# Optimization experiments

Measured on AMD Instinct MI355X. Metric: run time of the kernel, lower is better.

The kernel has to match this reference:

```python
import jax, jax.numpy as jnp
import numpy as np

NUM_HEADS = 32
NUM_KV_HEADS = 8
HEAD_DIM = 128


def setup_inputs() -> dict:
    key = jax.random.key(0)
    ks = jax.random.split(key, 5)
    B, S, H = 2, 2048, 4096
    Dq = NUM_HEADS * HEAD_DIM      # 4096
    Dkv = NUM_KV_HEADS * HEAD_DIM  # 1024
    return {
        "hidden_states": jax.random.normal(ks[0], (B, S, H), jnp.float32),
        "w_q": jax.random.normal(ks[1], (H, Dq), jnp.float32) * 0.02,
        "w_k": jax.random.normal(ks[2], (H, Dkv), jnp.float32) * 0.02,
        "w_v": jax.random.normal(ks[3], (H, Dkv), jnp.float32) * 0.02,
        "w_o": jax.random.normal(ks[4], (Dq, H), jnp.float32) * 0.02,
    }


def reference(hidden_states, w_q, w_k, w_v, w_o):
    # GQA causal attention, prefill path (no KV cache, RoPE is a no-op in source).
    B, S, _ = hidden_states.shape
    Hq, Hkv, D = NUM_HEADS, NUM_KV_HEADS, HEAD_DIM
    g = Hq // Hkv  # kv groups
    scale = D ** -0.5

    q = (hidden_states @ w_q).reshape(B, S, Hkv, g, D)  # [B,S,Hkv,g,D]
    k = (hidden_states @ w_k).reshape(B, S, Hkv, D)     # [B,S,Hkv,D]
    v = (hidden_states @ w_v).reshape(B, S, Hkv, D)

    # repeat_kv expressed as grouped einsum (avoids materializing repeated K/V)
    scores = jnp.einsum('bqhgd,bkhd->bhgqk', q, k) * scale  # [B,Hkv,g,S,S]
    causal = jnp.tril(jnp.ones((S, S), dtype=bool))
    scores = jnp.where(causal, scores, -jnp.inf)
    probs = jax.nn.softmax(scores.astype(jnp.float32), axis=-1).astype(q.dtype)

    attn = jnp.einsum('bhgqk,bkhd->bqhgd', probs, v)  # [B,S,Hkv,g,D]
    attn = attn.reshape(B, S, Hq * D)
    return attn @ w_o
```

## Files before the change

kernel.cpp:

```cpp
#include <hip/hip_runtime.h>

typedef unsigned short u16;
typedef __attribute__((ext_vector_type(8))) short bf16x8;
typedef __attribute__((ext_vector_type(8))) unsigned short u16x8;
typedef __attribute__((ext_vector_type(4))) unsigned short u16x4;
typedef __attribute__((ext_vector_type(4))) float f32x4;

__device__ __forceinline__ u16 f2bf(float f) {
  union { float f; unsigned u; } v; v.f = f;
  unsigned r = v.u + 0x7fffu + ((v.u >> 16) & 1u);
  return (u16)(r >> 16);
}

__device__ __forceinline__ void gload16(const u16* g, u16* l) {
  __builtin_amdgcn_global_load_lds((const __attribute__((address_space(1))) void*)g,
                                   (__attribute__((address_space(3))) void*)l, 16, 0, 0);
}

__global__ __launch_bounds__(256) void cast_bf16_kern(const float* __restrict__ in,
                                                      u16* __restrict__ out, int n) {
  int i = (blockIdx.x * 256 + threadIdx.x) * 8;
  if (i >= n) return;
  float4 a = *(const float4*)(in + i);
  float4 b = *(const float4*)(in + i + 4);
  u16x8 r;
  r[0] = f2bf(a.x); r[1] = f2bf(a.y); r[2] = f2bf(a.z); r[3] = f2bf(a.w);
  r[4] = f2bf(b.x); r[5] = f2bf(b.y); r[6] = f2bf(b.z); r[7] = f2bf(b.w);
  *(u16x8*)(out + i) = r;
}

__global__ __launch_bounds__(256) void transpose_cast_kern(const float* __restrict__ in,
                                                           u16* __restrict__ out, int K, int N) {
  __shared__ float tile[64][65];
  int nbx = N >> 6;
  int n0 = (blockIdx.x % nbx) << 6;
  int k0 = (blockIdx.x / nbx) << 6;
  int tx = threadIdx.x & 15;
  int ty = threadIdx.x >> 4;
#pragma unroll
  for (int r = 0; r < 64; r += 16) {
    float4 v = *(const float4*)(in + (size_t)(k0 + ty + r) * N + n0 + tx * 4);
    tile[ty + r][tx * 4 + 0] = v.x;
    tile[ty + r][tx * 4 + 1] = v.y;
    tile[ty + r][tx * 4 + 2] = v.z;
    tile[ty + r][tx * 4 + 3] = v.w;
  }
  __syncthreads();
#pragma unroll
  for (int r = 0; r < 64; r += 16) {
    u16x4 o;
#pragma unroll
    for (int j = 0; j < 4; j++) o[j] = f2bf(tile[tx * 4 + j][ty + r]);
    *(u16x4*)(out + (size_t)(n0 + ty + r) * K + k0 + tx * 4) = o;
  }
}

#define PH_PRE()                                           \
  asm volatile("" ::: "memory");                           \
  __builtin_amdgcn_s_barrier();                            \
  asm volatile("" ::: "memory");                           \
  __builtin_amdgcn_s_setprio(1)

#define PH_POST()                                          \
  __builtin_amdgcn_s_setprio(0);                           \
  asm volatile("" ::: "memory");                           \
  __builtin_amdgcn_s_barrier();                            \
  asm volatile("" ::: "memory")

template <int MODE>
__global__ __launch_bounds__(512, 2) void gemm256(const u16* __restrict__ A,
                                                  const u16* __restrict__ Bt,
                                                  void* __restrict__ Cout,
                                                  int M, int N, int K) {
  __shared__ u16 lds[65536];
  const int tid = threadIdx.x;
  const int lane = tid & 63, w = tid >> 6;
  const int wm = w >> 2, wn = w & 3;
  const int li = lane & 15, lg = lane >> 4;
  const int NT = K >> 6;

  const int nbx = N >> 8;
  const int nwg = gridDim.x;
  const int swz = (blockIdx.x & 7) * (nwg >> 3) + (blockIdx.x >> 3);
  const int m0 = (swz / nbx) << 8;
  const int n0 = (swz % nbx) << 8;

  const int srow = w * 16 + (lane >> 3);
  const int scol = ((lane & 7) ^ (lane >> 3)) << 3;
  const u16* sA0 = A + (size_t)(m0 + srow) * K + scol;
  const u16* sA1 = A + (size_t)(m0 + 128 + srow) * K + scol;
  const u16* sB0 = Bt + (size_t)(n0 + srow) * K + scol;
  const u16* sB1 = Bt + (size_t)(n0 + 128 + srow) * K + scol;
  const size_t jK = (size_t)8 * K;
  u16* dA0 = lds + w * 1024;
  u16* dA1 = lds + 8192 + w * 1024;
  u16* dB0 = lds + 32768 + w * 1024;
  u16* dB1 = lds + 32768 + 8192 + w * 1024;

#define STG(sp, dp, t_) do {                                          \
    int db_ = (t_) & 1;                                               \
    gload16((sp) + (size_t)(t_) * 64, (dp) + db_ * 16384);            \
    gload16((sp) + (size_t)(t_) * 64 + jK, (dp) + db_ * 16384 + 512); \
  } while (0)

  STG(sA0, dA0, 0); STG(sA1, dA1, 0); STG(sB0, dB0, 0); STG(sB1, dB1, 0);
  STG(sA0, dA0, 1); STG(sA1, dA1, 1); STG(sB0, dB0, 1); STG(sB1, dB1, 1);
  asm volatile("s_waitcnt vmcnt(8)" ::: "memory");
  __builtin_amdgcn_s_barrier();
  asm volatile("" ::: "memory");

  f32x4 acc[8][4];
#pragma unroll
  for (int m = 0; m < 8; m++)
#pragma unroll
    for (int n = 0; n < 4; n++) acc[m][n] = (f32x4){0.f, 0.f, 0.f, 0.f};

  const int xsw = (li & 7) << 3;
  const int k0o = (lg * 8) ^ xsw;
  const int k1o = (32 + lg * 8) ^ xsw;
  const u16* aBase = lds + wm * 8192;
  const u16* bBase = lds + 32768 + (wn >> 1) * 8192;
  const int brow0 = (wn & 1) * 64;

  bf16x8 a[4][2], b[4][2];

  for (int t = 0; t < NT; ++t) {
    const int db = t & 1;
    const u16* Ab = aBase + db * 16384;
    const u16* Bb = bBase + db * 16384;

#pragma unroll
    for (int mf = 0; mf < 4; mf++) {
      int r = mf * 16 + li;
      a[mf][0] = *(const bf16x8*)(Ab + r * 64 + k0o);
      a[mf][1] = *(const bf16x8*)(Ab + r * 64 + k1o);
    }
#pragma unroll
    for (int nf = 0; nf < 2; nf++) {
      int r = brow0 + nf * 16 + li;
      b[nf][0] = *(const bf16x8*)(Bb + r * 64 + k0o);
      b[nf][1] = *(const bf16x8*)(Bb + r * 64 + k1o);
    }
    PH_PRE();
#pragma unroll
    for (int mf = 0; mf < 4; mf++)
#pragma unroll
      for (int nf = 0; nf < 2; nf++) {
        acc[mf][nf] = __builtin_amdgcn_mfma_f32_16x16x32_bf16(a[mf][0], b[nf][0], acc[mf][nf], 0, 0, 0);
        acc[mf][nf] = __builtin_amdgcn_mfma_f32_16x16x32_bf16(a[mf][1], b[nf][1], acc[mf][nf], 0, 0, 0);
      }
    PH_POST();

#pragma unroll
    for (int nf = 2; nf < 4; nf++) {
      int r = brow0 + nf * 16 + li;
      b[nf][0] = *(const bf16x8*)(Bb + r * 64 + k0o);
      b[nf][1] = *(const bf16x8*)(Bb + r * 64 + k1o);
    }
    PH_PRE();
#pragma unroll
    for (int mf = 0; mf < 4; mf++)
#pragma unroll
      for (int nf = 2; nf < 4; nf++) {
        acc[mf][nf] = __builtin_amdgcn_mfma_f32_16x16x32_bf16(a[mf][0], b[nf][0], acc[mf][nf], 0, 0, 0);
        acc[mf][nf] = __builtin_amdgcn_mfma_f32_16x16x32_bf16(a[mf][1], b[nf][1], acc[mf][nf], 0, 0, 0);
      }
    PH_POST();

#pragma unroll
    for (int mf = 0; mf < 4; mf++) {
      int r = (mf + 4) * 16 + li;
      a[mf][0] = *(const bf16x8*)(Ab + r * 64 + k0o);
      a[mf][1] = *(const bf16x8*)(Ab + r * 64 + k1o);
    }
    if (t + 2 < NT) { STG(sB0, dB0, t + 2); STG(sB1, dB1, t + 2); }
    PH_PRE();
#pragma unroll
    for (int mf = 0; mf < 4; mf++)
#pragma unroll
      for (int nf = 2; nf < 4; nf++) {
        acc[mf + 4][nf] = __builtin_amdgcn_mfma_f32_16x16x32_bf16(a[mf][0], b[nf][0], acc[mf + 4][nf], 0, 0, 0);
        acc[mf + 4][nf] = __builtin_amdgcn_mfma_f32_16x16x32_bf16(a[mf][1], b[nf][1], acc[mf + 4][nf], 0, 0, 0);
      }
    PH_POST();

    if (t + 2 < NT) { STG(sA0, dA0, t + 2); STG(sA1, dA1, t + 2); }
    PH_PRE();
#pragma unroll
    for (int mf = 0; mf < 4; mf++)
#pragma unroll
      for (int nf = 0; nf < 2; nf++) {
        acc[mf + 4][nf] = __builtin_amdgcn_mfma_f32_16x16x32_bf16(a[mf][0], b[nf][0], acc[mf + 4][nf], 0, 0, 0);
        acc[mf + 4][nf] = __builtin_amdgcn_mfma_f32_16x16x32_bf16(a[mf][1], b[nf][1], acc[mf + 4][nf], 0, 0, 0);
      }
    __builtin_amdgcn_s_setprio(0);
    if (t < NT - 2) {
      asm volatile("s_waitcnt vmcnt(8)" ::: "memory");
    } else {
      asm volatile("s_waitcnt vmcnt(0)" ::: "memory");
    }
    __builtin_amdgcn_s_barrier();
    asm volatile("" ::: "memory");
  }

#pragma unroll
  for (int mf = 0; mf < 8; mf++)
#pragma unroll
    for (int nf = 0; nf < 4; nf++)
#pragma unroll
      for (int r = 0; r < 4; r++) {
        int gm = m0 + wm * 128 + mf * 16 + lg * 4 + r;
        int gn = n0 + wn * 64 + nf * 16 + li;
        if (MODE == 0)
          ((u16*)Cout)[(size_t)gm * N + gn] = f2bf(acc[mf][nf][r]);
        else
          ((float*)Cout)[(size_t)gm * N + gn] = acc[mf][nf][r];
      }
#undef STG
}

__global__ __launch_bounds__(512, 2) void gemm_kv(const u16* __restrict__ A,
                                                  const u16* __restrict__ Bt,
                                                  u16* __restrict__ Kout,
                                                  u16* __restrict__ Vout) {
  __shared__ u16 lds[49152];
  const int tid = threadIdx.x;
  const int lane = tid & 63, w = tid >> 6;
  const int wm = w >> 2, wn = w & 3;
  const int li = lane & 15, lg = lane >> 4;
  const int K = 4096, NT = 64;

  const int swz = (blockIdx.x & 7) * 32 + (blockIdx.x >> 3);
  const int m0 = (swz >> 3) << 7;
  const int n0 = (swz & 7) << 8;

  const int srow = w * 16 + (lane >> 3);
  const int scol = ((lane & 7) ^ (lane >> 3)) << 3;
  const u16* sA  = A  + (size_t)(m0 + srow) * K + scol;
  const u16* sB0 = Bt + (size_t)(n0 + srow) * K + scol;
  const u16* sB1 = Bt + (size_t)(n0 + 128 + srow) * K + scol;
  const size_t jK = (size_t)8 * K;
  u16* dA  = lds + w * 1024;
  u16* dB0 = lds + 16384 + w * 1024;
  u16* dB1 = lds + 16384 + 8192 + w * 1024;

#define STGA(t_) do { int db_ = (t_) & 1;                                     \
    gload16(sA + (size_t)(t_) * 64, dA + db_ * 8192);                         \
    gload16(sA + (size_t)(t_) * 64 + jK, dA + db_ * 8192 + 512); } while (0)
#define STGB(t_) do { int db_ = (t_) & 1;                                     \
    gload16(sB0 + (size_t)(t_) * 64, dB0 + db_ * 16384);                      \
    gload16(sB0 + (size_t)(t_) * 64 + jK, dB0 + db_ * 16384 + 512);           \
    gload16(sB1 + (size_t)(t_) * 64, dB1 + db_ * 16384);                      \
    gload16(sB1 + (size_t)(t_) * 64 + jK, dB1 + db_ * 16384 + 512); } while (0)

  STGA(0); STGB(0); STGB(1);
  asm volatile("s_waitcnt vmcnt(4)" ::: "memory");
  __builtin_amdgcn_s_barrier();
  asm volatile("" ::: "memory");

  f32x4 acc[4][4];
#pragma unroll
  for (int m = 0; m < 4; m++)
#pragma unroll
    for (int n = 0; n < 4; n++) acc[m][n] = (f32x4){0.f, 0.f, 0.f, 0.f};

  const int xsw = (li & 7) << 3;
  const int k0o = (lg * 8) ^ xsw;
  const int k1o = (32 + lg * 8) ^ xsw;
  const int arow0 = wm * 64;
  const u16* bBase0 = lds + 16384 + (wn >> 1) * 8192;
  const int brow0 = (wn & 1) * 64;

  bf16x8 a[4][2], b[4][2];

  for (int t = 0; t < NT; ++t) {
    const int db = t & 1;
    const u16* Ab = lds + db * 8192;
    const u16* Bb = bBase0 + db * 16384;

#pragma unroll
    for (int mf = 0; mf < 2; mf++) {
      int r = arow0 + mf * 16 + li;
      a[mf][0] = *(const bf16x8*)(Ab + r * 64 + k0o);
      a[mf][1] = *(const bf16x8*)(Ab + r * 64 + k1o);
    }
#pragma unroll
    for (int nf = 0; nf < 4; nf++) {
      int r = brow0 + nf * 16 + li;
      b[nf][0] = *(const bf16x8*)(Bb + r * 64 + k0o);
      b[nf][1] = *(const bf16x8*)(Bb + r * 64 + k1o);
    }
    if (t + 1 < NT) STGA(t + 1);
    PH_PRE();
#pragma unroll
    for (int mf = 0; mf < 2; mf++)
#pragma unroll
      for (int nf = 0; nf < 4; nf++) {
        acc[mf][nf] = __builtin_amdgcn_mfma_f32_16x16x32_bf16(a[mf][0], b[nf][0], acc[mf][nf], 0, 0, 0);
        acc[mf][nf] = __builtin_amdgcn_mfma_f32_16x16x32_bf16(a[mf][1], b[nf][1], acc[mf][nf], 0, 0, 0);
      }
    PH_POST();

#pragma unroll
    for (int mf = 2; mf < 4; mf++) {
      int r = arow0 + mf * 16 + li;
      a[mf][0] = *(const bf16x8*)(Ab + r * 64 + k0o);
      a[mf][1] = *(const bf16x8*)(Ab + r * 64 + k1o);
    }
    if (t + 2 < NT) STGB(t + 2);
    PH_PRE();
#pragma unroll
    for (int mf = 2; mf < 4; mf++)
#pragma unroll
      for (int nf = 0; nf < 4; nf++) {
        acc[mf][nf] = __builtin_amdgcn_mfma_f32_16x16x32_bf16(a[mf][0], b[nf][0], acc[mf][nf], 0, 0, 0);
        acc[mf][nf] = __builtin_amdgcn_mfma_f32_16x16x32_bf16(a[mf][1], b[nf][1], acc[mf][nf], 0, 0, 0);
      }
    __builtin_amdgcn_s_setprio(0);
    if (t < NT - 2) {
      asm volatile("s_waitcnt vmcnt(4)" ::: "memory");
    } else {
      asm volatile("s_waitcnt vmcnt(0)" ::: "memory");
    }
    __builtin_amdgcn_s_barrier();
    asm volatile("" ::: "memory");
  }

#pragma unroll
  for (int mf = 0; mf < 4; mf++)
#pragma unroll
    for (int nf = 0; nf < 4; nf++)
#pragma unroll
      for (int r = 0; r < 4; r++) {
        int gm = m0 + wm * 64 + mf * 16 + lg * 4 + r;
        int gn = n0 + wn * 64 + nf * 16 + li;
        float val = acc[mf][nf][r];
        if (gn < 1024) {
          Kout[(size_t)gm * 1024 + gn] = f2bf(val);
        } else {
          int c = gn - 1024;
          int b = gm >> 11, s = gm & 2047, kvh = c >> 7, d = c & 127;
          int s2 = (s & ~31) | (((s >> 2) & 3) << 3) | (((s >> 4) & 1) << 2) | (s & 3);
          Vout[(size_t)((b * 8 + kvh) * 128 + d) * 2048 + s2] = f2bf(val);
        }
      }
#undef STGA
#undef STGB
}

__global__ __launch_bounds__(256, 2) void flash_attn_kern(const u16* __restrict__ Qg,
                                                          const u16* __restrict__ Kg,
                                                          const u16* __restrict__ VT,
                                                          u16* __restrict__ Og) {
  const int bid = blockIdx.x;
  const int qt = 63 - (bid >> 4);
  const int gh = bid & 15;
  const int b = gh >> 3, kvh = gh & 7;
  const int tid = threadIdx.x;
  const int lane = tid & 63, w = tid >> 6;
  const int li = lane & 15, lg = lane >> 4;
  const int h = kvh * 4 + w;
  const int q0 = qt << 5;
  const int nt = (qt >> 1) + 1;

  __shared__ u16 Kbuf[2][8192];
  __shared__ u16 Vbuf[2][8192];

  bf16x8 qf[2][4];
  {
    const u16* qp = Qg + ((size_t)(b * 2048 + q0 + li)) * 4096 + h * 128 + lg * 8;
#pragma unroll
    for (int m = 0; m < 2; m++)
#pragma unroll
      for (int ks = 0; ks < 4; ks++)
        qf[m][ks] = *(const bf16x8*)(qp + (size_t)(m * 16) * 4096 + ks * 32);
  }

  const u16* ksrc[4];
  const u16* vsrc[4];
#pragma unroll
  for (int i = 0; i < 4; i++) {
    int c = w * 4 + i;
    int krow = c * 4 + (lane >> 4);
    int kinner = ((lane & 15) * 16) ^ ((krow & 7) << 4);
    ksrc[i] = Kg + (size_t)(b * 2048 + krow) * 1024 + kvh * 128 + (kinner >> 1);
    int vrow = c * 8 + (lane >> 3);
    int vinner = ((lane & 7) * 16) ^ ((vrow & 7) << 4);
    vsrc[i] = VT + (size_t)((b * 8 + kvh) * 128 + vrow) * 2048 + (vinner >> 1);
  }
#pragma unroll
  for (int i = 0; i < 4; i++) {
    int c = w * 4 + i;
    gload16(ksrc[i], &Kbuf[0][c * 512]);
    gload16(vsrc[i], &Vbuf[0][c * 512]);
    ksrc[i] += 64 * 1024;
    vsrc[i] += 64;
  }

  f32x4 oa[2][8];
#pragma unroll
  for (int m = 0; m < 2; m++)
#pragma unroll
    for (int n = 0; n < 8; n++) oa[m][n] = (f32x4){0.f, 0.f, 0.f, 0.f};
  f32x4 lacc[2];
  lacc[0] = (f32x4){0.f, 0.f, 0.f, 0.f};
  lacc[1] = (f32x4){0.f, 0.f, 0.f, 0.f};
  float mrun[2] = {-1e30f, -1e30f};

  const float scale = 0.08838834764831845f;
  bf16x8 onesf;
#pragma unroll
  for (int j = 0; j < 8; j++) onesf[j] = (short)0x3F80;

  asm volatile("s_waitcnt vmcnt(0)\n\ts_barrier" ::: "memory");

  for (int t = 0; t < nt; ++t) {
    const int cur = t & 1;
    const u16* KB = Kbuf[cur];
    const u16* VB = Vbuf[cur];
    if (t + 1 < nt) {
#pragma unroll
      for (int i = 0; i < 4; i++) {
        int c = w * 4 + i;
        gload16(ksrc[i], &Kbuf[cur ^ 1][c * 512]);
        gload16(vsrc[i], &Vbuf[cur ^ 1][c * 512]);
        ksrc[i] += 64 * 1024;
        vsrc[i] += 64;
      }
    }

    f32x4 sacc[2][4];
#pragma unroll
    for (int m = 0; m < 2; m++)
#pragma unroll
      for (int n = 0; n < 4; n++) sacc[m][n] = (f32x4){0.f, 0.f, 0.f, 0.f};
    __builtin_amdgcn_s_setprio(1);
#pragma unroll
    for (int n = 0; n < 4; n++) {
      int krow = n * 16 + li;
      const u16* kb = KB + krow * 128;
      int sw = (krow & 7) << 4;
#pragma unroll
      for (int ks = 0; ks < 4; ks++) {
        bf16x8 kf = *(const bf16x8*)(kb + (((ks * 64 + lg * 16) ^ sw) >> 1));
        sacc[0][n] = __builtin_amdgcn_mfma_f32_16x16x32_bf16(kf, qf[0][ks], sacc[0][n], 0, 0, 0);
        sacc[1][n] = __builtin_amdgcn_mfma_f32_16x16x32_bf16(kf, qf[1][ks], sacc[1][n], 0, 0, 0);
      }
    }
    __builtin_amdgcn_s_setprio(0);

#pragma unroll
    for (int m = 0; m < 2; m++)
#pragma unroll
      for (int n = 0; n < 4; n++)
#pragma unroll
        for (int r = 0; r < 4; r++) sacc[m][n][r] *= scale;
    if (t == nt - 1) {
      const int kv0 = t * 64;
#pragma unroll
      for (int m = 0; m < 2; m++) {
        int q = q0 + m * 16 + li;
#pragma unroll
        for (int n = 0; n < 4; n++)
#pragma unroll
          for (int r = 0; r < 4; r++)
            if (kv0 + n * 16 + lg * 4 + r > q) sacc[m][n][r] = -1e30f;
      }
    }

#pragma unroll
    for (int m = 0; m < 2; m++) {
      float mx = sacc[m][0][0];
#pragma unroll
      for (int n = 0; n < 4; n++)
#pragma unroll
        for (int r = 0; r < 4; r++) mx = fmaxf(mx, sacc[m][n][r]);
      mx = fmaxf(mx, __shfl_xor(mx, 16, 64));
      mx = fmaxf(mx, __shfl_xor(mx, 32, 64));
      float mnew = fmaxf(mrun[m], mx);
      float corr = __expf(mrun[m] - mnew);
      mrun[m] = mnew;
#pragma unroll
      for (int n = 0; n < 4; n++)
#pragma unroll
        for (int r = 0; r < 4; r++) sacc[m][n][r] = __expf(sacc[m][n][r] - mnew);
#pragma unroll
      for (int r = 0; r < 4; r++) lacc[m][r] *= corr;
#pragma unroll
      for (int n = 0; n < 8; n++)
#pragma unroll
        for (int r = 0; r < 4; r++) oa[m][n][r] *= corr;
    }

    bf16x8 pf[2][2];
#pragma unroll
    for (int m = 0; m < 2; m++)
#pragma unroll
      for (int kvs = 0; kvs < 2; kvs++) {
        u16x8 pw;
#pragma unroll
        for (int e = 0; e < 8; e++) pw[e] = f2bf(sacc[m][2 * kvs + (e >> 2)][e & 3]);
        pf[m][kvs] = *(bf16x8*)&pw;
      }

    __builtin_amdgcn_s_setprio(1);
#pragma unroll
    for (int kvs = 0; kvs < 2; kvs++) {
#pragma unroll
      for (int n = 0; n < 8; n++) {
        int vrow = n * 16 + li;
        bf16x8 vf = *(const bf16x8*)(VB + vrow * 64 +
                                     (((kvs * 64 + lg * 16) ^ ((vrow & 7) << 4)) >> 1));
        oa[0][n] = __builtin_amdgcn_mfma_f32_16x16x32_bf16(vf, pf[0][kvs], oa[0][n], 0, 0, 0);
        oa[1][n] = __builtin_amdgcn_mfma_f32_16x16x32_bf16(vf, pf[1][kvs], oa[1][n], 0, 0, 0);
      }
      lacc[0] = __builtin_amdgcn_mfma_f32_16x16x32_bf16(onesf, pf[0][kvs], lacc[0], 0, 0, 0);
      lacc[1] = __builtin_amdgcn_mfma_f32_16x16x32_bf16(onesf, pf[1][kvs], lacc[1], 0, 0, 0);
    }
    __builtin_amdgcn_s_setprio(0);

    asm volatile("s_waitcnt vmcnt(0)\n\ts_barrier" ::: "memory");
  }

#pragma unroll
  for (int m = 0; m < 2; m++) {
    float inv = 1.0f / lacc[m][0];
    u16* op = Og + (size_t)(b * 2048 + q0 + m * 16 + li) * 4096 + h * 128 + lg * 4;
#pragma unroll
    for (int n = 0; n < 8; n++) {
      u16x4 o;
#pragma unroll
      for (int r = 0; r < 4; r++) o[r] = f2bf(oa[m][n][r] * inv);
      *(u16x4*)(op + n * 16) = o;
    }
  }
}

extern "C" void kernel_launch(void* const* d_in, const int* in_sizes, int n_in,
                              void* d_out, int out_size, void* d_ws, size_t ws_size,
                              hipStream_t stream) {
  (void)in_sizes; (void)n_in; (void)out_size; (void)ws_size;
  const float* hs = (const float*)d_in[0];
  const float* wq = (const float*)d_in[1];
  const float* wk = (const float*)d_in[2];
  const float* wv = (const float*)d_in[3];
  const float* wo = (const float*)d_in[4];

  u16* ws   = (u16*)d_ws;
  u16* hs_b = ws;
  u16* wqT  = hs_b + 16777216;
  u16* wkT  = wqT + 16777216;
  u16* wvT  = wkT + 4194304;
  u16* woT  = wvT + 4194304;
  u16* Qb   = woT + 16777216;
  u16* Kb   = Qb + 16777216;
  u16* VTb  = Kb + 4194304;
  u16* attnb = VTb + 4194304;

  cast_bf16_kern<<<8192, 256, 0, stream>>>(hs, hs_b, 16777216);
  transpose_cast_kern<<<4096, 256, 0, stream>>>(wq, wqT, 4096, 4096);
  transpose_cast_kern<<<1024, 256, 0, stream>>>(wk, wkT, 4096, 1024);
  transpose_cast_kern<<<1024, 256, 0, stream>>>(wv, wvT, 4096, 1024);
  transpose_cast_kern<<<4096, 256, 0, stream>>>(wo, woT, 4096, 4096);

  gemm256<0><<<256, 512, 0, stream>>>(hs_b, wqT, Qb, 4096, 4096, 4096);
  gemm_kv<<<256, 512, 0, stream>>>(hs_b, wkT, Kb, VTb);

  flash_attn_kern<<<1024, 256, 0, stream>>>(Qb, Kb, VTb, attnb);

  gemm256<2><<<256, 512, 0, stream>>>(attnb, woT, (float*)d_out, 4096, 4096, 4096);
}
```

Measured before the change: 482.0 us.

## Split GEMM into dedicated producer loader waves and consumer MFMA waves

The 256x256 GEMM now launches 768 threads: 4 producer waves issue all global-to-LDS loads for the next K tile, and 8 consumer waves only do LDS reads and MFMAs. The two groups stay in step with one barrier per K step, which replaces the interleaved per-phase barriers and loads inside the compute waves. The aim is to take load issue off the MFMA waves and simplify their schedule. In exchange, occupancy drops to one block per CU, prefetch depth falls from two tiles ahead to one, and producers wait for vmcnt(0) every step, which may expose memory latency.

```diff
diff --git a/kernel.cpp b/kernel.cpp
--- a/kernel.cpp
+++ b/kernel.cpp
@@ -16,6 +16,9 @@
   __builtin_amdgcn_global_load_lds((const __attribute__((address_space(1))) void*)g,
                                    (__attribute__((address_space(3))) void*)l, 16, 0, 0);
 }
+
+#define FENCE() asm volatile("" ::: "memory")
+#define BARRIER() do { FENCE(); __builtin_amdgcn_s_barrier(); FENCE(); } while (0)
 
 __global__ __launch_bounds__(256) void cast_bf16_kern(const float* __restrict__ in,
                                                       u16* __restrict__ out, int n) {
@@ -55,28 +58,14 @@
   }
 }
 
-#define PH_PRE()                                           \
-  asm volatile("" ::: "memory");                           \
-  __builtin_amdgcn_s_barrier();                            \
-  asm volatile("" ::: "memory");                           \
-  __builtin_amdgcn_s_setprio(1)
-
-#define PH_POST()                                          \
-  __builtin_amdgcn_s_setprio(0);                           \
-  asm volatile("" ::: "memory");                           \
-  __builtin_amdgcn_s_barrier();                            \
-  asm volatile("" ::: "memory")
-
 template <int MODE>
-__global__ __launch_bounds__(512, 2) void gemm256(const u16* __restrict__ A,
+__global__ __launch_bounds__(768, 1) void gemm256(const u16* __restrict__ A,
                                                   const u16* __restrict__ Bt,
                                                   void* __restrict__ Cout,
                                                   int M, int N, int K) {
   __shared__ u16 lds[65536];
   const int tid = threadIdx.x;
   const int lane = tid & 63, w = tid >> 6;
-  const int wm = w >> 2, wn = w & 3;
-  const int li = lane & 15, lg = lane >> 4;
   const int NT = K >> 6;
 
   const int nbx = N >> 8;
@@ -85,29 +74,43 @@
   const int m0 = (swz / nbx) << 8;
   const int n0 = (swz % nbx) << 8;
 
-  const int srow = w * 16 + (lane >> 3);
-  const int scol = ((lane & 7) ^ (lane >> 3)) << 3;
-  const u16* sA0 = A + (size_t)(m0 + srow) * K + scol;
-  const u16* sA1 = A + (size_t)(m0 + 128 + srow) * K + scol;
-  const u16* sB0 = Bt + (size_t)(n0 + srow) * K + scol;
-  const u16* sB1 = Bt + (size_t)(n0 + 128 + srow) * K + scol;
-  const size_t jK = (size_t)8 * K;
-  u16* dA0 = lds + w * 1024;
-  u16* dA1 = lds + 8192 + w * 1024;
-  u16* dB0 = lds + 32768 + w * 1024;
-  u16* dB1 = lds + 32768 + 8192 + w * 1024;
-
-#define STG(sp, dp, t_) do {                                          \
-    int db_ = (t_) & 1;                                               \
-    gload16((sp) + (size_t)(t_) * 64, (dp) + db_ * 16384);            \
-    gload16((sp) + (size_t)(t_) * 64 + jK, (dp) + db_ * 16384 + 512); \
-  } while (0)
-
-  STG(sA0, dA0, 0); STG(sA1, dA1, 0); STG(sB0, dB0, 0); STG(sB1, dB1, 0);
-  STG(sA0, dA0, 1); STG(sA1, dA1, 1); STG(sB0, dB0, 1); STG(sB1, dB1, 1);
-  asm volatile("s_waitcnt vmcnt(8)" ::: "memory");
-  __builtin_amdgcn_s_barrier();
-  asm volatile("" ::: "memory");
+  if (w >= 8) {
+    const int pw = w - 8;
+    const int scol = ((lane & 7) ^ (lane >> 3)) << 3;
+    const int rb = pw * 32 + (lane >> 3);
+    const u16* gA0 = A + (size_t)(m0 + rb) * K + scol;
+    const u16* gA1 = A + (size_t)(m0 + 128 + rb) * K + scol;
+    const u16* gB0 = Bt + (size_t)(n0 + rb) * K + scol;
+    const u16* gB1 = Bt + (size_t)(n0 + 128 + rb) * K + scol;
+    const size_t g8K = (size_t)8 * K;
+    u16* const dA0 = lds + pw * 2048;
+    u16* const dA1 = lds + 8192 + pw * 2048;
+    u16* const dB0 = lds + 32768 + pw * 2048;
+    u16* const dB1 = lds + 32768 + 8192 + pw * 2048;
+
+#define STGP(t_) do { int db_ = (t_) & 1; size_t ko_ = (size_t)(t_) * 64;   \
+    _Pragma("unroll")                                                       \
+    for (int g_ = 0; g_ < 4; g_++) {                                        \
+      gload16(gA0 + ko_ + g_ * g8K, dA0 + db_ * 16384 + g_ * 512);          \
+      gload16(gA1 + ko_ + g_ * g8K, dA1 + db_ * 16384 + g_ * 512);          \
+      gload16(gB0 + ko_ + g_ * g8K, dB0 + db_ * 16384 + g_ * 512);          \
+      gload16(gB1 + ko_ + g_ * g8K, dB1 + db_ * 16384 + g_ * 512);          \
+    } } while (0)
+
+    STGP(0);
+    asm volatile("s_waitcnt vmcnt(0)" ::: "memory");
+    BARRIER();
+    for (int t = 0; t < NT; ++t) {
+      if (t + 1 < NT) STGP(t + 1);
+      asm volatile("s_waitcnt vmcnt(0)" ::: "memory");
+      BARRIER();
+    }
+#undef STGP
+    return;
+  }
+
+  const int wm = w >> 2, wn = w & 3;
+  const int li = lane & 15, lg = lane >> 4;
 
   f32x4 acc[8][4];
 #pragma unroll
@@ -124,6 +127,8 @@
 
   bf16x8 a[4][2], b[4][2];
 
+  BARRIER();
+
   for (int t = 0; t < NT; ++t) {
     const int db = t & 1;
     const u16* Ab = aBase + db * 16384;
@@ -141,7 +146,7 @@
       b[nf][0] = *(const bf16x8*)(Bb + r * 64 + k0o);
       b[nf][1] = *(const bf16x8*)(Bb + r * 64 + k1o);
     }
-    PH_PRE();
+    __builtin_amdgcn_s_setprio(1);
 #pragma unroll
     for (int mf = 0; mf < 4; mf++)
 #pragma unroll
@@ -149,7 +154,7 @@
         acc[mf][nf] = __builtin_amdgcn_mfma_f32_16x16x32_bf16(a[mf][0], b[nf][0], acc[mf][nf], 0, 0, 0);
         acc[mf][nf] = __builtin_amdgcn_mfma_f32_16x16x32_bf16(a[mf][1], b[nf][1], acc[mf][nf], 0, 0, 0);
       }
-    PH_POST();
+    __builtin_amdgcn_s_setprio(0);
 
 #pragma unroll
     for (int nf = 2; nf < 4; nf++) {
@@ -157,7 +162,7 @@
       b[nf][0] = *(const bf16x8*)(Bb + r * 64 + k0o);
       b[nf][1] = *(const bf16x8*)(Bb + r * 64 + k1o);
     }
-    PH_PRE();
+    __builtin_amdgcn_s_setprio(1);
 #pragma unroll
     for (int mf = 0; mf < 4; mf++)
 #pragma unroll
@@ -165,7 +170,7 @@
         acc[mf][nf] = __builtin_amdgcn_mfma_f32_16x16x32_bf16(a[mf][0], b[nf][0], acc[mf][nf], 0, 0, 0);
         acc[mf][nf] = __builtin_amdgcn_mfma_f32_16x16x32_bf16(a[mf][1], b[nf][1], acc[mf][nf], 0, 0, 0);
       }
-    PH_POST();
+    __builtin_amdgcn_s_setprio(0);
 
 #pragma unroll
     for (int mf = 0; mf < 4; mf++) {
@@ -173,34 +178,17 @@
       a[mf][0] = *(const bf16x8*)(Ab + r * 64 + k0o);
       a[mf][1] = *(const bf16x8*)(Ab + r * 64 + k1o);
     }
-    if (t + 2 < NT) { STG(sB0, dB0, t + 2); STG(sB1, dB1, t + 2); }
-    PH_PRE();
+    __builtin_amdgcn_s_setprio(1);
 #pragma unroll
     for (int mf = 0; mf < 4; mf++)
 #pragma unroll
-      for (int nf = 2; nf < 4; nf++) {
+      for (int nf = 0; nf < 4; nf++) {
         acc[mf + 4][nf] = __builtin_amdgcn_mfma_f32_16x16x32_bf16(a[mf][0], b[nf][0], acc[mf + 4][nf], 0, 0, 0);
         acc[mf + 4][nf] = __builtin_amdgcn_mfma_f32_16x16x32_bf16(a[mf][1], b[nf][1], acc[mf + 4][nf], 0, 0, 0);
       }
-    PH_POST();
-
-    if (t + 2 < NT) { STG(sA0, dA0, t + 2); STG(sA1, dA1, t + 2); }
-    PH_PRE();
-#pragma unroll
-    for (int mf = 0; mf < 4; mf++)
-#pragma unroll
-      for (int nf = 0; nf < 2; nf++) {
-        acc[mf + 4][nf] = __builtin_amdgcn_mfma_f32_16x16x32_bf16(a[mf][0], b[nf][0], acc[mf + 4][nf], 0, 0, 0);
-        acc[mf + 4][nf] = __builtin_amdgcn_mfma_f32_16x16x32_bf16(a[mf][1], b[nf][1], acc[mf + 4][nf], 0, 0, 0);
-      }
     __builtin_amdgcn_s_setprio(0);
-    if (t < NT - 2) {
-      asm volatile("s_waitcnt vmcnt(8)" ::: "memory");
-    } else {
-      asm volatile("s_waitcnt vmcnt(0)" ::: "memory");
-    }
-    __builtin_amdgcn_s_barrier();
-    asm volatile("" ::: "memory");
+
+    BARRIER();
   }
 
 #pragma unroll
@@ -216,8 +204,19 @@
         else
           ((float*)Cout)[(size_t)gm * N + gn] = acc[mf][nf][r];
       }
-#undef STG
-}
+}
+
+#define PH_PRE()                                           \
+  asm volatile("" ::: "memory");                           \
+  __builtin_amdgcn_s_barrier();                            \
+  asm volatile("" ::: "memory");                           \
+  __builtin_amdgcn_s_setprio(1)
+
+#define PH_POST()                                          \
+  __builtin_amdgcn_s_setprio(0);                           \
+  asm volatile("" ::: "memory");                           \
+  __builtin_amdgcn_s_barrier();                            \
+  asm volatile("" ::: "memory")
 
 __global__ __launch_bounds__(512, 2) void gemm_kv(const u16* __restrict__ A,
                                                   const u16* __restrict__ Bt,
@@ -563,10 +562,10 @@
   transpose_cast_kern<<<1024, 256, 0, stream>>>(wv, wvT, 4096, 1024);
   transpose_cast_kern<<<4096, 256, 0, stream>>>(wo, woT, 4096, 4096);
 
-  gemm256<0><<<256, 512, 0, stream>>>(hs_b, wqT, Qb, 4096, 4096, 4096);
+  gemm256<0><<<256, 768, 0, stream>>>(hs_b, wqT, Qb, 4096, 4096, 4096);
   gemm_kv<<<256, 512, 0, stream>>>(hs_b, wkT, Kb, VTb);
 
   flash_attn_kern<<<1024, 256, 0, stream>>>(Qb, Kb, VTb, attnb);
 
-  gemm256<2><<<256, 512, 0, stream>>>(attnb, woT, (float*)d_out, 4096, 4096, 4096);
-}
+  gemm256<2><<<256, 768, 0, stream>>>(attnb, woT, (float*)d_out, 4096, 4096, 4096);
+}
```

After: 922.9 us. 91.5% more time.
